# Kernel tuning notes

Measured on AMD Instinct MI355X. Metric: run time of the kernel, lower is better.

Reference implementation:

```python
import jax, jax.numpy as jnp
import numpy as np

D_OUT = 1536
BN_EPS = 1e-5


def _batchnorm(h, g, b):
    # torch BatchNorm1d in training mode: biased batch stats
    m = jnp.mean(h, axis=0)
    v = jnp.var(h, axis=0)
    return g * (h - m) * jax.lax.rsqrt(v + BN_EPS) + b


def setup_inputs() -> dict:
    key = jax.random.key(0)
    ks = jax.random.split(key, 16)
    B = 8192
    d0, d1, dib = 1024, 768, 1024
    s = lambda d: (2.0 / d) ** 0.5
    inp = {
        "x0": jax.random.normal(ks[0], (B, d0), jnp.float32),
        "x1": jax.random.normal(ks[1], (B, d1), jnp.float32),
        "x_ib": jax.random.normal(ks[2], (B, dib), jnp.float32),
        # 7 expert projections per source (Reaction_Head_mini modeled as linear proj)
        "pW0": jax.random.normal(ks[3], (7, d0, D_OUT), jnp.float32) * s(d0),
        "pb0": jnp.zeros((7, D_OUT), jnp.float32),
        "pW1": jax.random.normal(ks[4], (7, d1, D_OUT), jnp.float32) * s(d1),
        "pb1": jnp.zeros((7, D_OUT), jnp.float32),
        "pWib": jax.random.normal(ks[5], (7, dib, D_OUT), jnp.float32) * s(dib),
        "pbib": jnp.zeros((7, D_OUT), jnp.float32),
        # MOE_Router_Sig: Linear(1024,512)+BN+relu -> Linear(512,100)+BN+tanh -> Linear(100,3)
        "rw1": jax.random.normal(ks[6], (d0, 512), jnp.float32) * s(d0),
        "rb1": jnp.zeros((512,), jnp.float32),
        "rg1": jnp.ones((512,), jnp.float32),
        "rbt1": jnp.zeros((512,), jnp.float32),
        "rw2": jax.random.normal(ks[7], (512, 100), jnp.float32) * s(512),
        "rb2": jnp.zeros((100,), jnp.float32),
        "rg2": jnp.ones((100,), jnp.float32),
        "rbt2": jnp.zeros((100,), jnp.float32),
        "rw3": jax.random.normal(ks[8], (100, 3), jnp.float32) * s(100),
        "rb3": jnp.zeros((3,), jnp.float32),
    }
    return inp


def reference(x0, x1, x_ib, pW0, pb0, pW1, pb1, pWib, pbib,
              rw1, rb1, rg1, rbt1, rw2, rb2, rg2, rbt2, rw3, rb3):
    # ---- expert projections (torch.no_grad in original) ----
    e0 = jnp.einsum('bd,kdf->bkf', x0, pW0) + pb0      # [B,7,1536]
    e1 = jnp.einsum('bd,kdf->bkf', x1, pW1) + pb1      # [B,7,1536]
    eib = jnp.einsum('bd,kdf->bkf', x_ib, pWib) + pbib # [B,7,1536]
    ex = jnp.concatenate([e0, e1, eib], axis=1)        # [B,21,1536]
    B = ex.shape[0]
    # seg_mean with segment length 7 -> [B,3,1536]
    ex = ex.reshape(B, 3, 7, D_OUT).mean(axis=2)
    ex = jax.lax.stop_gradient(ex)
    # ---- router: MOE_Router_Sig(x0) -> sigmoid -> softmax ----
    h = _batchnorm(x0 @ rw1 + rb1, rg1, rbt1)
    h = jax.nn.relu(h)
    h = _batchnorm(h @ rw2 + rb2, rg2, rbt2)
    h = jnp.tanh(h)
    logits = jax.nn.sigmoid(h @ rw3 + rb3)             # [B,3]
    w = jax.nn.softmax(logits, axis=-1)                # [B,3]
    # ---- weighted combine + L2 normalize ----
    out = jnp.sum(ex * w[:, :, None], axis=1)          # [B,1536]
    out = out / jnp.linalg.norm(out, axis=-1, keepdims=True).clip(1e-12)
    return out
```

## Files before the change

kernel.cpp:

```cpp
#include <hip/hip_runtime.h>
#include <stdint.h>

typedef __attribute__((ext_vector_type(8))) short short8;
typedef __attribute__((ext_vector_type(4))) float floatx4;

__device__ inline unsigned short f2bf(float f) {
    unsigned int u = __float_as_uint(f);
    u += 0x7fffu + ((u >> 16) & 1u);
    return (unsigned short)(u >> 16);
}

__device__ void avg_transpose_tile(const float* __restrict__ src,
                                   unsigned short* __restrict__ dst,
                                   int E, int K, int Nsrc, int Ndst, int ldb,
                                   float scale, int tile_x, int tile_y) {
    __shared__ float tile[32][33];
    const int tid = threadIdx.x;
    const int tx = tid & 31;
    const int ty = tid >> 5;
    const int kb = tile_x * 32;
    const int nb = tile_y * 32;
#pragma unroll
    for (int p = 0; p < 4; ++p) {
        int kl = ty + p * 8;
        int k = kb + kl;
        int n = nb + tx;
        float s = 0.f;
        if (k < K && n < Nsrc) {
            for (int e = 0; e < E; ++e)
                s += src[(size_t)e * K * Nsrc + (size_t)k * Nsrc + n];
        }
        tile[kl][tx] = s * scale;
    }
    __syncthreads();
#pragma unroll
    for (int p = 0; p < 4; ++p) {
        int nl = ty + p * 8;
        int n = nb + nl;
        int k = kb + tx;
        if (n < Ndst && k < K)
            dst[(size_t)n * ldb + k] = f2bf(tile[tx][nl]);
    }
}

__global__ __launch_bounds__(256) void prep(
    const float* __restrict__ pW0, const float* __restrict__ pW1,
    const float* __restrict__ pWib, const float* __restrict__ rw1,
    const float* __restrict__ rw2, const float* __restrict__ pb0,
    const float* __restrict__ pb1, const float* __restrict__ pbib,
    const float* __restrict__ x0,
    unsigned short* __restrict__ Wmt, unsigned short* __restrict__ rw1t,
    unsigned short* __restrict__ rw2t, float* __restrict__ bm0,
    float* __restrict__ bm1, float* __restrict__ bm2,
    float* __restrict__ stats_zero, unsigned short* __restrict__ X0b) {
    int id = blockIdx.x;
    int tid = threadIdx.x;
    if (id < 1536) {
        avg_transpose_tile(pW0, Wmt + 0, 7, 1024, 1536, 1536, 2816, 1.f / 7.f,
                           id % 32, id / 32);
    } else if (id < 2688) {
        int t = id - 1536;
        avg_transpose_tile(pW1, Wmt + 1024, 7, 768, 1536, 1536, 2816, 1.f / 7.f,
                           t % 24, t / 24);
    } else if (id < 4224) {
        int t = id - 2688;
        avg_transpose_tile(pWib, Wmt + 1792, 7, 1024, 1536, 1536, 2816,
                           1.f / 7.f, t % 32, t / 32);
    } else if (id < 4736) {
        int t = id - 4224;
        avg_transpose_tile(rw1, rw1t, 1, 1024, 512, 512, 1024, 1.f, t % 32,
                           t / 32);
    } else if (id < 4800) {
        int t = id - 4736;
        avg_transpose_tile(rw2, rw2t, 1, 512, 100, 128, 512, 1.f, t % 16,
                           t / 16);
    } else if (id < 4806) {
        int i = (id - 4800) * 256 + tid;
        if (i < 1536) {
            float s0 = 0.f, s1 = 0.f, s2 = 0.f;
            for (int e = 0; e < 7; ++e) {
                s0 += pb0[e * 1536 + i];
                s1 += pb1[e * 1536 + i];
                s2 += pbib[e * 1536 + i];
            }
            const float inv = 1.f / 7.f;
            bm0[i] = s0 * inv; bm1[i] = s1 * inv; bm2[i] = s2 * inv;
        }
    } else if (id < 4807) {
        for (int i = tid; i < 1280; i += 256) stats_zero[i] = 0.f;
    } else {
        int base = (id - 4807) * 1024;
#pragma unroll
        for (int k = 0; k < 4; ++k) {
            int i = base + k * 256 + tid;
            float4 v = ((const float4*)x0)[i];
            ushort4 o;
            o.x = f2bf(v.x); o.y = f2bf(v.y); o.z = f2bf(v.z); o.w = f2bf(v.w);
            ((ushort4*)X0b)[i] = o;
        }
    }
}

template <int MODE>
__global__ __launch_bounds__(256) void gemm_bt(
    const unsigned short* __restrict__ A, const unsigned short* __restrict__ Bt,
    float* __restrict__ C, int K, int Nreal, int ldc,
    const float* __restrict__ bias, float* __restrict__ sum,
    float* __restrict__ sumsq, const float* __restrict__ w0,
    const float* __restrict__ w1, const float* __restrict__ w2,
    const float* __restrict__ bm0, const float* __restrict__ bm1,
    const float* __restrict__ bm2) {
    __shared__ __align__(16) unsigned short As[128 * 32];
    __shared__ __align__(16) unsigned short Bs[128 * 32];
    const int tid = threadIdx.x;
    const int lane = tid & 63;
    const int wv = tid >> 6;
    const int bm_off = blockIdx.x * 128;
    const int bn_off = blockIdx.y * 128;
    const int wm = (wv & 1) * 64;
    const int wn = (wv >> 1) * 64;
    floatx4 acc[4][4];
#pragma unroll
    for (int i = 0; i < 4; ++i)
#pragma unroll
        for (int j = 0; j < 4; ++j) acc[i][j] = (floatx4){0.f, 0.f, 0.f, 0.f};

    const int quad = lane >> 4;
    const int lrow = lane & 15;
    const int srow = lane >> 2;
    const int scol = (lane & 3) * 8;

    const unsigned short* Ag = A + (size_t)bm_off * K;
    const unsigned short* Bg = Bt + (size_t)bn_off * K;

    for (int k0 = 0; k0 < K; k0 += 32) {
#pragma unroll
        for (int r = 0; r < 2; ++r) {
            int chunk = r * 4 + wv;
            {
                const unsigned short* gp =
                    Ag + (size_t)(chunk * 16 + srow) * K + (k0 + scol);
                __builtin_amdgcn_global_load_lds(
                    (const __attribute__((address_space(1))) void*)gp,
                    (__attribute__((address_space(3))) void*)(As + chunk * 512),
                    16, 0, 0);
            }
            {
                const unsigned short* gp =
                    Bg + (size_t)(chunk * 16 + srow) * K + (k0 + scol);
                __builtin_amdgcn_global_load_lds(
                    (const __attribute__((address_space(1))) void*)gp,
                    (__attribute__((address_space(3))) void*)(Bs + chunk * 512),
                    16, 0, 0);
            }
        }
        __syncthreads();
        short8 af[4], bfr[4];
#pragma unroll
        for (int i = 0; i < 4; ++i)
            af[i] = *(const short8*)(As + (wm + i * 16 + lrow) * 32 + quad * 8);
#pragma unroll
        for (int j = 0; j < 4; ++j)
            bfr[j] = *(const short8*)(Bs + (wn + j * 16 + lrow) * 32 + quad * 8);
#pragma unroll
        for (int i = 0; i < 4; ++i)
#pragma unroll
            for (int j = 0; j < 4; ++j)
                acc[i][j] = __builtin_amdgcn_mfma_f32_16x16x32_bf16(
                    af[i], bfr[j], acc[i][j], 0, 0, 0);
        __syncthreads();
    }

    if (MODE == 1) {
#pragma unroll
        for (int i = 0; i < 4; ++i) {
#pragma unroll
            for (int r = 0; r < 4; ++r) {
                int m = bm_off + wm + i * 16 + quad * 4 + r;
                float wb0 = w0[m], wb1 = w1[m], wb2 = w2[m];
#pragma unroll
                for (int j = 0; j < 4; ++j) {
                    int n = bn_off + wn + j * 16 + lrow;
                    float v = acc[i][j][r] + wb0 * bm0[n] + wb1 * bm1[n] +
                              wb2 * bm2[n];
                    C[(size_t)m * ldc + n] = v;
                }
            }
        }
    } else {
#pragma unroll
        for (int j = 0; j < 4; ++j) {
            int n = bn_off + wn + j * 16 + lrow;
            bool nok = (n < Nreal);
            float bv = nok ? bias[n] : 0.f;
            float s = 0.f, ss = 0.f;
#pragma unroll
            for (int i = 0; i < 4; ++i) {
#pragma unroll
                for (int r = 0; r < 4; ++r) {
                    float v = acc[i][j][r] + bv;
                    int m = bm_off + wm + i * 16 + quad * 4 + r;
                    if (nok) C[(size_t)m * ldc + n] = v;
                    s += v; ss += v * v;
                }
            }
            s += __shfl_xor(s, 16); s += __shfl_xor(s, 32);
            ss += __shfl_xor(ss, 16); ss += __shfl_xor(ss, 32);
            if (quad == 0 && nok) {
                atomicAdd(&sum[n], s);
                atomicAdd(&sumsq[n], ss);
            }
        }
    }
}

__global__ __launch_bounds__(512, 2) void gemm256(
    const unsigned short* __restrict__ A, const unsigned short* __restrict__ Bt,
    float* __restrict__ C, int K, int ldc,
    const float* __restrict__ w0, const float* __restrict__ w1,
    const float* __restrict__ w2, const float* __restrict__ g0,
    const float* __restrict__ g1, const float* __restrict__ g2) {
    __shared__ __align__(16) unsigned short lds[57344];
    unsigned short* Asb = lds;
    unsigned short* Bsb = lds + 32768;

    const int tid = threadIdx.x;
    const int lane = tid & 63;
    const int wv = tid >> 6;
    const int wm = wv >> 2;
    const int wn = wv & 3;
    const int quad = lane >> 4;
    const int lrow = lane & 15;

    int id = blockIdx.y * 32 + blockIdx.x;
    id = (id & 7) * 32 + (id >> 3);
    const int row0 = (id & 31) * 256;
    const int col0 = (id >> 5) * 192;

    size_t srcA[2];
#pragma unroll
    for (int c = 0; c < 2; ++c) {
        int idx = c * 512 + tid;
        int r = idx >> 2;
        int sl = (idx & 3) ^ ((r >> 1) & 3);
        srcA[c] = (size_t)(row0 + r) * K + sl * 8;
    }
    size_t srcB16;
    {
        int r = tid >> 2;
        int sl = (tid & 3) ^ ((r >> 1) & 3);
        srcB16 = (size_t)(col0 + r) * K + sl * 8;
    }
    size_t srcB4[2];
#pragma unroll
    for (int d = 0; d < 2; ++d) {
        int byteoff = d * 2048 + tid * 4;
        int r = 128 + (byteoff >> 6);
        int sl = ((byteoff >> 4) & 3) ^ ((r >> 1) & 3);
        srcB4[d] = (size_t)(col0 + r) * K + sl * 8 + ((tid & 3) << 1);
    }

    auto stageA = [&](int kt, int buf) {
        const int k0 = kt * 32;
#pragma unroll
        for (int c = 0; c < 2; ++c) {
            __builtin_amdgcn_global_load_lds(
                (const __attribute__((address_space(1))) void*)(A + srcA[c] + k0),
                (__attribute__((address_space(3))) void*)(Asb + buf * 8192 +
                                                         c * 4096 + wv * 512),
                16, 0, 0);
        }
    };
    auto stageB = [&](int kt, int buf) {
        const int k0 = kt * 32;
        __builtin_amdgcn_global_load_lds(
            (const __attribute__((address_space(1))) void*)(Bt + srcB16 + k0),
            (__attribute__((address_space(3))) void*)(Bsb + buf * 6144 +
                                                     wv * 512),
            16, 0, 0);
#pragma unroll
        for (int d = 0; d < 2; ++d) {
            __builtin_amdgcn_global_load_lds(
                (const __attribute__((address_space(1))) void*)(Bt + srcB4[d] + k0),
                (__attribute__((address_space(3))) void*)(Bsb + buf * 6144 +
                                                         4096 + d * 1024 +
                                                         wv * 128),
                4, 0, 0);
        }
    };

    floatx4 acc[8][3];
#pragma unroll
    for (int i = 0; i < 8; ++i)
#pragma unroll
        for (int j = 0; j < 3; ++j) acc[i][j] = (floatx4){0.f, 0.f, 0.f, 0.f};

    const int NT = K >> 5;
    stageA(0, 0); stageB(0, 0);
    stageA(1, 1); stageB(1, 1);
    stageA(2, 2); stageB(2, 2);
    asm volatile("s_waitcnt vmcnt(10)" ::: "memory");
    asm volatile("s_barrier" ::: "memory");

    for (int t = 0; t < NT; ++t) {
        const int buf = t & 3;
        const int nb = (t + 3) & 3;
        const bool pre = (t + 3 < NT);
        const unsigned short* Ab = Asb + buf * 8192;
        const unsigned short* Bb = Bsb + buf * 6144;

        if (pre) stageA(t + 3, nb);
        short8 bfr[3];
#pragma unroll
        for (int j = 0; j < 3; ++j) {
            int r = wn * 48 + j * 16 + lrow;
            bfr[j] = *(const short8*)(Bb + r * 32 +
                                      ((quad ^ ((r >> 1) & 3)) << 3));
        }
        short8 af0[4];
#pragma unroll
        for (int i = 0; i < 4; ++i) {
            int r = wm * 128 + i * 16 + lrow;
            af0[i] = *(const short8*)(Ab + r * 32 +
                                      ((quad ^ ((r >> 1) & 3)) << 3));
        }
        __builtin_amdgcn_s_setprio(1);
#pragma unroll
        for (int i = 0; i < 4; ++i)
#pragma unroll
            for (int j = 0; j < 3; ++j)
                acc[i][j] = __builtin_amdgcn_mfma_f32_16x16x32_bf16(
                    af0[i], bfr[j], acc[i][j], 0, 0, 0);
        __builtin_amdgcn_s_setprio(0);

        if (pre) stageB(t + 3, nb);
        short8 af1[4];
#pragma unroll
        for (int i = 0; i < 4; ++i) {
            int r = wm * 128 + 64 + i * 16 + lrow;
            af1[i] = *(const short8*)(Ab + r * 32 +
                                      ((quad ^ ((r >> 1) & 3)) << 3));
        }
        __builtin_amdgcn_s_setprio(1);
#pragma unroll
        for (int i = 0; i < 4; ++i)
#pragma unroll
            for (int j = 0; j < 3; ++j)
                acc[4 + i][j] = __builtin_amdgcn_mfma_f32_16x16x32_bf16(
                    af1[i], bfr[j], acc[4 + i][j], 0, 0, 0);
        __builtin_amdgcn_s_setprio(0);

        if (t + 1 < NT) {
            if (t + 3 < NT)
                asm volatile("s_waitcnt vmcnt(10)" ::: "memory");
            else if (t + 2 < NT)
                asm volatile("s_waitcnt vmcnt(5)" ::: "memory");
            else
                asm volatile("s_waitcnt vmcnt(0)" ::: "memory");
            asm volatile("s_barrier" ::: "memory");
        }
    }

#pragma unroll
    for (int ii = 0; ii < 8; ++ii) {
#pragma unroll
        for (int r = 0; r < 4; ++r) {
            int m = row0 + wm * 128 + ii * 16 + quad * 4 + r;
            float a0 = w0[m], a1 = w1[m], a2 = w2[m];
#pragma unroll
            for (int j = 0; j < 3; ++j) {
                int n = col0 + wn * 48 + j * 16 + lrow;
                C[(size_t)m * ldc + n] =
                    acc[ii][j][r] + a0 * g0[n] + a1 * g1[n] + a2 * g2[n];
            }
        }
    }
}

__global__ __launch_bounds__(256) void bn_relu_pack(
    const float* __restrict__ h, unsigned short* __restrict__ out,
    const float* __restrict__ sum, const float* __restrict__ sumsq,
    const float* __restrict__ g, const float* __restrict__ b) {
    __shared__ float sc[512], sh[512];
    const float invB = 1.f / 8192.f;
    for (int c = threadIdx.x; c < 512; c += 256) {
        float m = sum[c] * invB;
        float v = sumsq[c] * invB - m * m;
        float s = g[c] * rsqrtf(v + 1e-5f);
        sc[c] = s;
        sh[c] = b[c] - m * s;
    }
    __syncthreads();
    int base = blockIdx.x * 4096;
#pragma unroll
    for (int k = 0; k < 16; ++k) {
        int i = base + k * 256 + threadIdx.x;
        int c4 = (i & 127) * 4;
        float4 v = ((const float4*)h)[i];
        ushort4 o;
        o.x = f2bf(fmaxf(v.x * sc[c4 + 0] + sh[c4 + 0], 0.f));
        o.y = f2bf(fmaxf(v.y * sc[c4 + 1] + sh[c4 + 1], 0.f));
        o.z = f2bf(fmaxf(v.z * sc[c4 + 2] + sh[c4 + 2], 0.f));
        o.w = f2bf(fmaxf(v.w * sc[c4 + 3] + sh[c4 + 3], 0.f));
        ((ushort4*)out)[i] = o;
    }
}

__global__ __launch_bounds__(128) void router_tail(
    const float* __restrict__ h2, const float* __restrict__ sum,
    const float* __restrict__ sumsq, const float* __restrict__ g,
    const float* __restrict__ b, const float* __restrict__ rw3,
    const float* __restrict__ rb3, float* __restrict__ w0,
    float* __restrict__ w1, float* __restrict__ w2) {
    __shared__ float sc[100], sh[100], w3[300], b3[3];
    int tid = threadIdx.x;
    const float invB = 1.f / 8192.f;
    if (tid < 100) {
        float m = sum[tid] * invB;
        float v = sumsq[tid] * invB - m * m;
        float s = g[tid] * rsqrtf(v + 1e-5f);
        sc[tid] = s;
        sh[tid] = b[tid] - m * s;
    }
    for (int i = tid; i < 300; i += 128) w3[i] = rw3[i];
    if (tid < 3) b3[tid] = rb3[tid];
    __syncthreads();
    int bi = blockIdx.x * 128 + tid;
    float l0 = b3[0], l1 = b3[1], l2 = b3[2];
    const float* hr = h2 + (size_t)bi * 100;
    for (int k = 0; k < 100; ++k) {
        float t = tanhf(hr[k] * sc[k] + sh[k]);
        l0 += t * w3[k * 3 + 0];
        l1 += t * w3[k * 3 + 1];
        l2 += t * w3[k * 3 + 2];
    }
    l0 = 1.f / (1.f + expf(-l0));
    l1 = 1.f / (1.f + expf(-l1));
    l2 = 1.f / (1.f + expf(-l2));
    float mx = fmaxf(l0, fmaxf(l1, l2));
    float e0 = expf(l0 - mx), e1 = expf(l1 - mx), e2 = expf(l2 - mx);
    float inv = 1.f / (e0 + e1 + e2);
    w0[bi] = e0 * inv; w1[bi] = e1 * inv; w2[bi] = e2 * inv;
}

__global__ __launch_bounds__(256) void pack_xp(
    const float* __restrict__ x0, const float* __restrict__ x1,
    const float* __restrict__ xib, const float* __restrict__ w0,
    const float* __restrict__ w1, const float* __restrict__ w2,
    unsigned short* __restrict__ Xp) {
    int i = blockIdx.x * blockDim.x + threadIdx.x;
    if (i >= 8192 * 704) return;
    int b = i / 704;
    int g = i % 704;
    const float* src;
    float w;
    int col;
    if (g < 256)      { src = x0 + (size_t)b * 1024 + g * 4;          w = w0[b]; col = g * 4; }
    else if (g < 448) { src = x1 + (size_t)b * 768 + (g - 256) * 4;   w = w1[b]; col = 1024 + (g - 256) * 4; }
    else              { src = xib + (size_t)b * 1024 + (g - 448) * 4; w = w2[b]; col = 1792 + (g - 448) * 4; }
    float4 v = *(const float4*)src;
    ushort4 o;
    o.x = f2bf(v.x * w); o.y = f2bf(v.y * w);
    o.z = f2bf(v.z * w); o.w = f2bf(v.w * w);
    *(ushort4*)(Xp + (size_t)b * 2816 + col) = o;
}

__global__ __launch_bounds__(256) void l2norm_rows(float* __restrict__ out) {
    int wv = threadIdx.x >> 6;
    int lane = threadIdx.x & 63;
    int row = blockIdx.x * 4 + wv;
    float4* rp = (float4*)(out + (size_t)row * 1536);
    float4 v[6];
    float ss = 0.f;
#pragma unroll
    for (int t = 0; t < 6; ++t) {
        v[t] = rp[lane + t * 64];
        ss += v[t].x * v[t].x + v[t].y * v[t].y + v[t].z * v[t].z + v[t].w * v[t].w;
    }
#pragma unroll
    for (int o = 32; o > 0; o >>= 1) ss += __shfl_xor(ss, o);
    float inv = 1.f / fmaxf(sqrtf(ss), 1e-12f);
#pragma unroll
    for (int t = 0; t < 6; ++t) {
        v[t].x *= inv; v[t].y *= inv; v[t].z *= inv; v[t].w *= inv;
        rp[lane + t * 64] = v[t];
    }
}

extern "C" void kernel_launch(void* const* d_in, const int* in_sizes, int n_in,
                              void* d_out, int out_size, void* d_ws,
                              size_t ws_size, hipStream_t stream) {
    (void)in_sizes; (void)n_in; (void)out_size; (void)ws_size;
    const float* x0   = (const float*)d_in[0];
    const float* x1   = (const float*)d_in[1];
    const float* xib  = (const float*)d_in[2];
    const float* pW0  = (const float*)d_in[3];
    const float* pb0  = (const float*)d_in[4];
    const float* pW1  = (const float*)d_in[5];
    const float* pb1  = (const float*)d_in[6];
    const float* pWib = (const float*)d_in[7];
    const float* pbib = (const float*)d_in[8];
    const float* rw1  = (const float*)d_in[9];
    const float* rb1  = (const float*)d_in[10];
    const float* rg1  = (const float*)d_in[11];
    const float* rbt1 = (const float*)d_in[12];
    const float* rw2  = (const float*)d_in[13];
    const float* rb2  = (const float*)d_in[14];
    const float* rg2  = (const float*)d_in[15];
    const float* rbt2 = (const float*)d_in[16];
    const float* rw3  = (const float*)d_in[17];
    const float* rb3  = (const float*)d_in[18];
    float* out = (float*)d_out;

    char* ws = (char*)d_ws;
    unsigned short* Wmt = (unsigned short*)(ws);
    char* stats = ws + 8650752;
    float* sum1   = (float*)(stats + 0);
    float* sumsq1 = (float*)(stats + 2048);
    float* sum2   = (float*)(stats + 4096);
    float* sumsq2 = (float*)(stats + 4608);
    float* bm0    = (float*)(stats + 10240);
    float* bm1    = (float*)(stats + 16384);
    float* bm2    = (float*)(stats + 22528);
    float* w0p    = (float*)(stats + 28672);
    float* w1p    = (float*)(stats + 61440);
    float* w2p    = (float*)(stats + 94208);
    unsigned short* rw1t = (unsigned short*)(ws + 8781824);
    unsigned short* rw2t = (unsigned short*)(ws + 9830400);
    char* R5 = ws + 9961472;
    unsigned short* X0b = (unsigned short*)(R5);
    float* h1           = (float*)(R5 + 16777216);
    unsigned short* h1n = (unsigned short*)(R5 + 33554432);
    float* h2           = (float*)(R5 + 41943040);
    unsigned short* Xp  = (unsigned short*)(R5);

    prep<<<6855, 256, 0, stream>>>(pW0, pW1, pWib, rw1, rw2, pb0, pb1, pbib, x0,
                                   Wmt, rw1t, rw2t, bm0, bm1, bm2,
                                   (float*)stats, X0b);
    gemm_bt<2><<<dim3(64, 4), 256, 0, stream>>>(
        X0b, rw1t, h1, 1024, 512, 512, rb1, sum1, sumsq1,
        nullptr, nullptr, nullptr, nullptr, nullptr, nullptr);
    bn_relu_pack<<<256, 256, 0, stream>>>(h1, h1n, sum1, sumsq1, rg1, rbt1);
    gemm_bt<2><<<dim3(64, 1), 256, 0, stream>>>(
        h1n, rw2t, h2, 512, 100, 100, rb2, sum2, sumsq2,
        nullptr, nullptr, nullptr, nullptr, nullptr, nullptr);
    router_tail<<<64, 128, 0, stream>>>(h2, sum2, sumsq2, rg2, rbt2, rw3, rb3,
                                        w0p, w1p, w2p);
    pack_xp<<<22528, 256, 0, stream>>>(x0, x1, xib, w0p, w1p, w2p, Xp);
    gemm256<<<dim3(32, 8), 512, 0, stream>>>(Xp, Wmt, out, 2816, 1536,
                                             w0p, w1p, w2p, bm0, bm1, bm2);
    l2norm_rows<<<2048, 256, 0, stream>>>(out);
}
```

Baseline: 421.7 us.

## Reuse bf16 x0 in final GEMM and apply router weight to accumulator

The final GEMM now reads its A operand from three separate bf16 buffers: the already-converted x0 from prep, plus newly packed weighted x1 and x_ib. It no longer uses a single packed 2816-wide Xp. The w0 row weight is applied by scaling the accumulator after the x0 segment, which avoids rewriting x0 scaled by w0. This removes a third of the packing kernel's reads and writes. The block-to-tile mapping is also changed to group rows by XCD, and the unused MODE 1 path is removed. The trade-off is a branchy A staging path and an extra scaling pass inside the k-loop.

```diff
diff --git a/kernel.cpp b/kernel.cpp
--- a/kernel.cpp
+++ b/kernel.cpp
@@ -106,10 +106,7 @@
     const unsigned short* __restrict__ A, const unsigned short* __restrict__ Bt,
     float* __restrict__ C, int K, int Nreal, int ldc,
     const float* __restrict__ bias, float* __restrict__ sum,
-    float* __restrict__ sumsq, const float* __restrict__ w0,
-    const float* __restrict__ w1, const float* __restrict__ w2,
-    const float* __restrict__ bm0, const float* __restrict__ bm1,
-    const float* __restrict__ bm2) {
+    float* __restrict__ sumsq) {
     __shared__ __align__(16) unsigned short As[128 * 32];
     __shared__ __align__(16) unsigned short Bs[128 * 32];
     const int tid = threadIdx.x;
@@ -171,23 +168,7 @@
         __syncthreads();
     }
 
-    if (MODE == 1) {
-#pragma unroll
-        for (int i = 0; i < 4; ++i) {
-#pragma unroll
-            for (int r = 0; r < 4; ++r) {
-                int m = bm_off + wm + i * 16 + quad * 4 + r;
-                float wb0 = w0[m], wb1 = w1[m], wb2 = w2[m];
-#pragma unroll
-                for (int j = 0; j < 4; ++j) {
-                    int n = bn_off + wn + j * 16 + lrow;
-                    float v = acc[i][j][r] + wb0 * bm0[n] + wb1 * bm1[n] +
-                              wb2 * bm2[n];
-                    C[(size_t)m * ldc + n] = v;
-                }
-            }
-        }
-    } else {
+    {
 #pragma unroll
         for (int j = 0; j < 4; ++j) {
             int n = bn_off + wn + j * 16 + lrow;
@@ -215,8 +196,9 @@
 }
 
 __global__ __launch_bounds__(512, 2) void gemm256(
-    const unsigned short* __restrict__ A, const unsigned short* __restrict__ Bt,
-    float* __restrict__ C, int K, int ldc,
+    const unsigned short* __restrict__ A0, const unsigned short* __restrict__ A1,
+    const unsigned short* __restrict__ A2, const unsigned short* __restrict__ Bt,
+    float* __restrict__ C, int ldc,
     const float* __restrict__ w0, const float* __restrict__ w1,
     const float* __restrict__ w2, const float* __restrict__ g0,
     const float* __restrict__ g1, const float* __restrict__ g2) {
@@ -232,24 +214,22 @@
     const int quad = lane >> 4;
     const int lrow = lane & 15;
 
-    int id = blockIdx.y * 32 + blockIdx.x;
-    id = (id & 7) * 32 + (id >> 3);
-    const int row0 = (id & 31) * 256;
-    const int col0 = (id >> 5) * 192;
-
-    size_t srcA[2];
-#pragma unroll
-    for (int c = 0; c < 2; ++c) {
-        int idx = c * 512 + tid;
-        int r = idx >> 2;
-        int sl = (idx & 3) ^ ((r >> 1) & 3);
-        srcA[c] = (size_t)(row0 + r) * K + sl * 8;
-    }
+    int b = blockIdx.y * 32 + blockIdx.x;
+    const int xcd = b & 7;
+    const int loc = b >> 3;
+    const int row0 = (xcd * 4 + (loc & 3)) * 256;
+    const int col0 = (loc >> 2) * 192;
+
+    const int rA = tid >> 2;
+    const int slA = (tid & 3) ^ ((rA >> 1) & 3);
+    const size_t sA0 = (size_t)(row0 + rA) * 1024 + slA * 8;
+    const size_t sA1 = (size_t)(row0 + rA) * 768 + slA * 8;
+
     size_t srcB16;
     {
         int r = tid >> 2;
         int sl = (tid & 3) ^ ((r >> 1) & 3);
-        srcB16 = (size_t)(col0 + r) * K + sl * 8;
+        srcB16 = (size_t)(col0 + r) * 2816 + sl * 8;
     }
     size_t srcB4[2];
 #pragma unroll
@@ -257,22 +237,39 @@
         int byteoff = d * 2048 + tid * 4;
         int r = 128 + (byteoff >> 6);
         int sl = ((byteoff >> 4) & 3) ^ ((r >> 1) & 3);
-        srcB4[d] = (size_t)(col0 + r) * K + sl * 8 + ((tid & 3) << 1);
+        srcB4[d] = (size_t)(col0 + r) * 2816 + sl * 8 + ((tid & 3) << 1);
     }
 
     auto stageA = [&](int kt, int buf) {
-        const int k0 = kt * 32;
-#pragma unroll
-        for (int c = 0; c < 2; ++c) {
-            __builtin_amdgcn_global_load_lds(
-                (const __attribute__((address_space(1))) void*)(A + srcA[c] + k0),
-                (__attribute__((address_space(3))) void*)(Asb + buf * 8192 +
-                                                         c * 4096 + wv * 512),
-                16, 0, 0);
+        unsigned short* d0 = Asb + buf * 8192 + wv * 512;
+        if (kt < 32) {
+            const unsigned short* g = A0 + (size_t)kt * 32;
+            __builtin_amdgcn_global_load_lds(
+                (const __attribute__((address_space(1))) void*)(g + sA0),
+                (__attribute__((address_space(3))) void*)d0, 16, 0, 0);
+            __builtin_amdgcn_global_load_lds(
+                (const __attribute__((address_space(1))) void*)(g + sA0 + 128 * 1024),
+                (__attribute__((address_space(3))) void*)(d0 + 4096), 16, 0, 0);
+        } else if (kt < 56) {
+            const unsigned short* g = A1 + (size_t)(kt - 32) * 32;
+            __builtin_amdgcn_global_load_lds(
+                (const __attribute__((address_space(1))) void*)(g + sA1),
+                (__attribute__((address_space(3))) void*)d0, 16, 0, 0);
+            __builtin_amdgcn_global_load_lds(
+                (const __attribute__((address_space(1))) void*)(g + sA1 + 128 * 768),
+                (__attribute__((address_space(3))) void*)(d0 + 4096), 16, 0, 0);
+        } else {
+            const unsigned short* g = A2 + (size_t)(kt - 56) * 32;
+            __builtin_amdgcn_global_load_lds(
+                (const __attribute__((address_space(1))) void*)(g + sA0),
+                (__attribute__((address_space(3))) void*)d0, 16, 0, 0);
+            __builtin_amdgcn_global_load_lds(
+                (const __attribute__((address_space(1))) void*)(g + sA0 + 128 * 1024),
+                (__attribute__((address_space(3))) void*)(d0 + 4096), 16, 0, 0);
         }
     };
     auto stageB = [&](int kt, int buf) {
-        const int k0 = kt * 32;
+        const size_t k0 = (size_t)kt * 32;
         __builtin_amdgcn_global_load_lds(
             (const __attribute__((address_space(1))) void*)(Bt + srcB16 + k0),
             (__attribute__((address_space(3))) void*)(Bsb + buf * 6144 +
@@ -295,7 +292,7 @@
 #pragma unroll
         for (int j = 0; j < 3; ++j) acc[i][j] = (floatx4){0.f, 0.f, 0.f, 0.f};
 
-    const int NT = K >> 5;
+    const int NT = 88;
     stageA(0, 0); stageB(0, 0);
     stageA(1, 1); stageB(1, 1);
     stageA(2, 2); stageB(2, 2);
@@ -349,6 +346,18 @@
                 acc[4 + i][j] = __builtin_amdgcn_mfma_f32_16x16x32_bf16(
                     af1[i], bfr[j], acc[4 + i][j], 0, 0, 0);
         __builtin_amdgcn_s_setprio(0);
+
+        if (t == 31) {
+#pragma unroll
+            for (int ii = 0; ii < 8; ++ii) {
+#pragma unroll
+                for (int r = 0; r < 4; ++r) {
+                    float f = w0[row0 + wm * 128 + ii * 16 + quad * 4 + r];
+#pragma unroll
+                    for (int j = 0; j < 3; ++j) acc[ii][j][r] *= f;
+                }
+            }
+        }
 
         if (t + 1 < NT) {
             if (t + 3 < NT)
@@ -443,26 +452,34 @@
     w0[bi] = e0 * inv; w1[bi] = e1 * inv; w2[bi] = e2 * inv;
 }
 
-__global__ __launch_bounds__(256) void pack_xp(
-    const float* __restrict__ x0, const float* __restrict__ x1,
-    const float* __restrict__ xib, const float* __restrict__ w0,
+__global__ __launch_bounds__(256) void pack1ib(
+    const float* __restrict__ x1, const float* __restrict__ xib,
     const float* __restrict__ w1, const float* __restrict__ w2,
-    unsigned short* __restrict__ Xp) {
-    int i = blockIdx.x * blockDim.x + threadIdx.x;
-    if (i >= 8192 * 704) return;
-    int b = i / 704;
-    int g = i % 704;
-    const float* src;
-    float w;
-    int col;
-    if (g < 256)      { src = x0 + (size_t)b * 1024 + g * 4;          w = w0[b]; col = g * 4; }
-    else if (g < 448) { src = x1 + (size_t)b * 768 + (g - 256) * 4;   w = w1[b]; col = 1024 + (g - 256) * 4; }
-    else              { src = xib + (size_t)b * 1024 + (g - 448) * 4; w = w2[b]; col = 1792 + (g - 448) * 4; }
-    float4 v = *(const float4*)src;
-    ushort4 o;
-    o.x = f2bf(v.x * w); o.y = f2bf(v.y * w);
-    o.z = f2bf(v.z * w); o.w = f2bf(v.w * w);
-    *(ushort4*)(Xp + (size_t)b * 2816 + col) = o;
+    unsigned short* __restrict__ X1b, unsigned short* __restrict__ Xib) {
+    int i0 = blockIdx.x * 1024 + threadIdx.x;
+#pragma unroll
+    for (int k = 0; k < 4; ++k) {
+        int i = i0 + k * 256;
+        int b = i / 448;
+        int g = i % 448;
+        float w;
+        const float* src;
+        unsigned short* dst;
+        if (g < 192) {
+            w = w1[b];
+            src = x1 + (size_t)b * 768 + g * 4;
+            dst = X1b + (size_t)b * 768 + g * 4;
+        } else {
+            w = w2[b];
+            src = xib + (size_t)b * 1024 + (g - 192) * 4;
+            dst = Xib + (size_t)b * 1024 + (g - 192) * 4;
+        }
+        float4 v = *(const float4*)src;
+        ushort4 o;
+        o.x = f2bf(v.x * w); o.y = f2bf(v.y * w);
+        o.z = f2bf(v.z * w); o.w = f2bf(v.w * w);
+        *(ushort4*)dst = o;
+    }
 }
 
 __global__ __launch_bounds__(256) void l2norm_rows(float* __restrict__ out) {
@@ -532,22 +549,21 @@
     float* h1           = (float*)(R5 + 16777216);
     unsigned short* h1n = (unsigned short*)(R5 + 33554432);
     float* h2           = (float*)(R5 + 41943040);
-    unsigned short* Xp  = (unsigned short*)(R5);
+    unsigned short* X1b = (unsigned short*)(R5 + 16777216);
+    unsigned short* Xib = (unsigned short*)(R5 + 29360128);
 
     prep<<<6855, 256, 0, stream>>>(pW0, pW1, pWib, rw1, rw2, pb0, pb1, pbib, x0,
                                    Wmt, rw1t, rw2t, bm0, bm1, bm2,
                                    (float*)stats, X0b);
     gemm_bt<2><<<dim3(64, 4), 256, 0, stream>>>(
-        X0b, rw1t, h1, 1024, 512, 512, rb1, sum1, sumsq1,
-        nullptr, nullptr, nullptr, nullptr, nullptr, nullptr);
+        X0b, rw1t, h1, 1024, 512, 512, rb1, sum1, sumsq1);
     bn_relu_pack<<<256, 256, 0, stream>>>(h1, h1n, sum1, sumsq1, rg1, rbt1);
     gemm_bt<2><<<dim3(64, 1), 256, 0, stream>>>(
-        h1n, rw2t, h2, 512, 100, 100, rb2, sum2, sumsq2,
-        nullptr, nullptr, nullptr, nullptr, nullptr, nullptr);
+        h1n, rw2t, h2, 512, 100, 100, rb2, sum2, sumsq2);
     router_tail<<<64, 128, 0, stream>>>(h2, sum2, sumsq2, rg2, rbt2, rw3, rb3,
                                         w0p, w1p, w2p);
-    pack_xp<<<22528, 256, 0, stream>>>(x0, x1, xib, w0p, w1p, w2p, Xp);
-    gemm256<<<dim3(32, 8), 512, 0, stream>>>(Xp, Wmt, out, 2816, 1536,
+    pack1ib<<<3584, 256, 0, stream>>>(x1, xib, w1p, w2p, X1b, Xib);
+    gemm256<<<dim3(32, 8), 512, 0, stream>>>(X0b, X1b, Xib, Wmt, out, 1536,
                                              w0p, w1p, w2p, bm0, bm1, bm2);
     l2norm_rows<<<2048, 256, 0, stream>>>(out);
 }
```

Result: no change. 416.7 us (median of 2 runs) (-1.2%).
